# Optimization experiments

Hardware: AMD Instinct MI355X
Metric: run time of the kernel (lower is better)

Reference implementation:

```python
import jax, jax.numpy as jnp
import numpy as np

EPS = 1e-5  # torch LayerNorm default

def layer_norm(x, scale, bias):
    m = jnp.mean(x, axis=-1, keepdims=True)
    v = jnp.var(x, axis=-1, keepdims=True)
    return (x - m) * jax.lax.rsqrt(v + EPS) * scale + bias

def setup_inputs() -> dict:
    key = jax.random.key(0)
    ks = jax.random.split(key, 8)
    B, N, E, D = 2, 50000, 262144, 256
    node_features = jax.random.normal(ks[0], (B, N, D), jnp.float32)
    edge_index = jax.random.randint(ks[1], (B, E, 2), 0, N)
    edge_relations = jax.random.normal(ks[2], (B, E, D), jnp.float32)
    edge_mask = jnp.ones((B, E), jnp.float32)
    sc = 1.0 / np.sqrt(D).astype(np.float32)
    rel_w = jax.random.normal(ks[3], (D, D), jnp.float32) * sc
    rel_b = jnp.zeros((D,), jnp.float32)
    norm_s = jnp.ones((D,), jnp.float32)
    norm_b = jnp.zeros((D,), jnp.float32)
    w1 = jax.random.normal(ks[4], (D, 4 * D), jnp.float32) * sc
    b1 = jnp.zeros((4 * D,), jnp.float32)
    w2 = jax.random.normal(ks[5], (4 * D, D), jnp.float32) * (1.0 / np.sqrt(4 * D).astype(np.float32))
    b2 = jnp.zeros((D,), jnp.float32)
    ffn_s = jnp.ones((D,), jnp.float32)
    ffn_b = jnp.zeros((D,), jnp.float32)
    return dict(node_features=node_features, edge_relations=edge_relations,
                edge_mask=edge_mask, rel_w=rel_w, rel_b=rel_b,
                norm_s=norm_s, norm_b=norm_b, w1=w1, b1=b1, w2=w2, b2=b2,
                ffn_s=ffn_s, ffn_b=ffn_b, edge_index=edge_index)

def reference(node_features, edge_relations, edge_mask, rel_w, rel_b,
              norm_s, norm_b, w1, b1, w2, b2, ffn_s, ffn_b, edge_index):
    B, N, D = node_features.shape
    bidx = jnp.arange(B)[:, None]                      # [B,1] batch index for gather/scatter
    src_idx = edge_index[:, :, 0]                      # [B,E]
    tgt_idx = edge_index[:, :, 1]                      # [B,E]
    src_features = node_features[bidx, src_idx]        # gather -> [B,E,D]
    rel_features = edge_relations @ rel_w + rel_b      # [B,E,D]
    messages = (src_features + rel_features) * edge_mask[..., None]
    aggregated = jnp.zeros_like(node_features).at[bidx, tgt_idx].add(messages)
    counts = jnp.zeros((B, N, 1), node_features.dtype).at[bidx, tgt_idx].add(edge_mask[..., None])
    counts = jnp.maximum(counts, 1.0)
    aggregated = aggregated / counts
    x = layer_norm(node_features + aggregated, norm_s, norm_b)
    h = jax.nn.gelu(x @ w1 + b1, approximate=False)    # torch GELU default = exact erf
    x = layer_norm(x + (h @ w2 + b2), ffn_s, ffn_b)
    return x
```

## Files before the change

### kernel.cpp

```cpp
#include <hip/hip_runtime.h>
#include <math.h>

#define Bn 2
#define Nn 50000
#define En 262144
#define Dn 256
#define Hn 1024
#define RTOT (Bn*Nn)
#define RHALF 50000

typedef short bf16x8 __attribute__((ext_vector_type(8)));
typedef float f32x4 __attribute__((ext_vector_type(4)));

__device__ __forceinline__ short f2b(float f) {
  unsigned u = __float_as_uint(f);
  u = u + 0x7fffu + ((u >> 16) & 1u);
  return (short)(u >> 16);
}

__device__ __forceinline__ float gelu_f(float v) {
  float x = fabsf(v) * 0.70710678118654752f;
  float t = __builtin_amdgcn_rcpf(1.0f + 0.47047f * x);
  float p = t*(0.3480242f + t*(-0.0958798f + t*0.7478556f));
  float er = 1.0f - p * __expf(-x*x);
  er = copysignf(er, v);
  return 0.5f * v * (1.0f + er);
}

__device__ __forceinline__ void gl16(const void* g, void* l) {
  __builtin_amdgcn_global_load_lds(
      (const __attribute__((address_space(1))) unsigned int*)g,
      (__attribute__((address_space(3))) unsigned int*)l, 16, 0, 0);
}

__global__ void __launch_bounds__(256) wconv(
    const float* __restrict__ relw, const float* __restrict__ w1,
    const float* __restrict__ w2, short* __restrict__ relwT,
    short* __restrict__ w1s, short* __restrict__ w2s) {
  int tid = blockIdx.x * 256 + threadIdx.x;
  if (tid < Dn*Dn) { int c = tid >> 8, k = tid & 255; relwT[tid] = f2b(relw[k*Dn + c]); }
  int t1 = tid - Dn*Dn;
  if (t1 >= 0 && t1 < Dn*Hn) {
    int kk = t1 >> 16, rem = t1 & 65535;
    int col = rem >> 6, kl = rem & 63;
    w1s[kk*65536 + col*64 + (kl ^ ((col & 7) << 3))] = f2b(w1[(kk*64 + kl)*Hn + col]);
  }
  int t2 = tid - Dn*Dn - Dn*Hn;
  if (t2 >= 0 && t2 < Hn*Dn) {
    int kk = t2 >> 14, rem = t2 & 16383;
    int col = rem >> 6, kl = rem & 63;
    w2s[kk*16384 + col*64 + (kl ^ ((col & 7) << 3))] = f2b(w2[(kk*64 + kl)*Dn + col]);
  }
}

__global__ void __launch_bounds__(256) histk(const int* __restrict__ ei, int* __restrict__ cnt) {
  int tid = blockIdx.x * 256 + threadIdx.x;
  if (tid >= Bn*En) return;
  int b = tid / En;
  int tgt = ei[tid*2 + 1];
  atomicAdd(&cnt[b*Nn + tgt], 1);
}

__global__ void __launch_bounds__(256) offsk(const int* __restrict__ cnt,
                                             int* __restrict__ offs, int* __restrict__ gtot) {
  int i = blockIdx.x * 256 + threadIdx.x;
  int lane = threadIdx.x & 63;
  int v = (i < RTOT) ? cnt[i] : 0;
  int s = v;
#pragma unroll
  for (int d = 1; d < 64; d <<= 1) {
    int t = __shfl_up(s, d, 64);
    if (lane >= d) s += t;
  }
  int base = 0;
  if (lane == 63) base = atomicAdd(gtot, s);
  base = __shfl(base, 63, 64);
  if (i < RTOT) offs[i] = base + s - v;
}

__global__ void __launch_bounds__(256) fillk(const int* __restrict__ ei, const int* __restrict__ offs,
                                             int* __restrict__ cursor, int* __restrict__ eids) {
  int tid = blockIdx.x * 256 + threadIdx.x;
  if (tid >= Bn*En) return;
  int b = tid / En, e = tid - b*En;
  int tgt = ei[tid*2 + 1];
  int node = b*Nn + tgt;
  int pos = atomicAdd(&cursor[node], 1);
  eids[offs[node] + pos] = e;
}

__global__ void __launch_bounds__(256) aggk(
    const float* __restrict__ nodef, const float* __restrict__ erel,
    const float* __restrict__ emask, const int* __restrict__ ei,
    const int* __restrict__ offs, const int* __restrict__ cnt,
    const int* __restrict__ eids,
    float* __restrict__ sumrel, float* __restrict__ cntf, float* __restrict__ outsrc) {
  int w = (blockIdx.x * 256 + threadIdx.x) >> 6;
  int lane = threadIdx.x & 63;
  if (w >= RTOT) return;
  int b = w / Nn;
  const size_t ebase = (size_t)b * En;
  const size_t nbase = (size_t)b * Nn;
  int s0 = offs[w], s1 = s0 + cnt[w];
  float r0=0,r1=0,r2=0,r3=0, a0=0,a1=0,a2=0,a3=0, cf=0;
  for (int base = s0; base < s1; base += 64) {
    int k = s1 - base; if (k > 64) k = 64;
    int e = 0, sr = 0; float m = 0.f;
    if (lane < k) {
      e  = eids[base + lane];
      sr = ei[(ebase + e)*2];
      m  = emask[ebase + e];
    }
    int e0 = __shfl(e, 0), sr0 = __shfl(sr, 0);
    float m0 = __shfl(m, 0);
    float4 rvA = *(const float4*)(erel  + (ebase + e0)*Dn + lane*4);
    float4 nvA = *(const float4*)(nodef + (nbase + sr0)*Dn + lane*4);
    for (int j = 0; j < k; j++) {
      float4 rvB = make_float4(0,0,0,0), nvB = make_float4(0,0,0,0);
      float m1 = 0.f;
      if (j + 1 < k) {
        int e1 = __shfl(e, j+1), sr1 = __shfl(sr, j+1);
        m1 = __shfl(m, j+1);
        rvB = *(const float4*)(erel  + (ebase + e1)*Dn + lane*4);
        nvB = *(const float4*)(nodef + (nbase + sr1)*Dn + lane*4);
      }
      r0 += rvA.x*m0; r1 += rvA.y*m0; r2 += rvA.z*m0; r3 += rvA.w*m0;
      a0 += nvA.x*m0; a1 += nvA.y*m0; a2 += nvA.z*m0; a3 += nvA.w*m0;
      cf += m0;
      rvA = rvB; nvA = nvB; m0 = m1;
    }
  }
  size_t ob = (size_t)w*Dn + lane*4;
  *(float4*)(sumrel + ob) = make_float4(r0,r1,r2,r3);
  *(float4*)(outsrc + ob) = make_float4(a0,a1,a2,a3);
  if (lane == 0) cntf[w] = cf;
}

template<int MR>
__device__ __forceinline__ void stageX(const float* __restrict__ src, char* lds, int row0, int tid) {
#pragma unroll
  for (int i = 0; i < MR*4; i++) {
    int flat = tid + 256*i;
    int r = flat >> 6, c4 = flat & 63;
    float4 v = *(const float4*)(src + (size_t)(row0 + r)*Dn + c4*4);
    short4 s; s.x=f2b(v.x); s.y=f2b(v.y); s.z=f2b(v.z); s.w=f2b(v.w);
    int byte = r*512 + ((c4*8) ^ ((r & 7) << 4));
    *(short4*)(lds + byte) = s;
  }
}

__device__ __forceinline__ bf16x8 ldsA(const char* lds, int r, int kb) {
  int byte = r*512 + (((kb)*2) ^ ((r & 7) << 4));
  return *(const bf16x8*)(lds + byte);
}

template<int MR>
__device__ __forceinline__ void ln_write(f32x4 (&acc)[MR][4], float* red,
    const float* __restrict__ sc, const float* __restrict__ bi,
    float* __restrict__ out, int row0, int lane, int wv) {
  constexpr int R = MR*16;
  int l15 = lane & 15, l4 = lane >> 4;
  int cols[4]; float sc_c[4], bi_c[4];
#pragma unroll
  for (int n = 0; n < 4; n++) {
    cols[n] = wv*64 + n*16 + l15;
    sc_c[n] = sc[cols[n]]; bi_c[n] = bi[cols[n]];
  }
  float s1[MR][4], s2[MR][4];
#pragma unroll
  for (int m = 0; m < MR; m++)
#pragma unroll
    for (int g = 0; g < 4; g++) {
      float a = 0.f, b = 0.f;
#pragma unroll
      for (int n = 0; n < 4; n++) { float p = acc[m][n][g]; a += p; b += p*p; }
#pragma unroll
      for (int d = 1; d < 16; d <<= 1) { a += __shfl_xor(a, d, 16); b += __shfl_xor(b, d, 16); }
      s1[m][g] = a; s2[m][g] = b;
    }
  if (l15 == 0) {
#pragma unroll
    for (int m = 0; m < MR; m++)
#pragma unroll
      for (int g = 0; g < 4; g++) {
        int r = m*16 + l4*4 + g;
        red[(wv*R + r)*2]     = s1[m][g];
        red[(wv*R + r)*2 + 1] = s2[m][g];
      }
  }
  __syncthreads();
#pragma unroll
  for (int m = 0; m < MR; m++)
#pragma unroll
    for (int g = 0; g < 4; g++) {
      int r = m*16 + l4*4 + g; int rg = row0 + r;
      float t1 = 0.f, t2 = 0.f;
#pragma unroll
      for (int u = 0; u < 4; u++) { t1 += red[(u*R + r)*2]; t2 += red[(u*R + r)*2 + 1]; }
      float mean = t1 * (1.0f/Dn);
      float var  = t2 * (1.0f/Dn) - mean*mean;
      float rstd = rsqrtf(var + 1e-5f);
#pragma unroll
      for (int n = 0; n < 4; n++)
        out[(size_t)rg*Dn + cols[n]] = (acc[m][n][g] - mean)*rstd*sc_c[n] + bi_c[n];
    }
}

__global__ void __launch_bounds__(256, 4) relln(
    const float* __restrict__ sumrel, const short* __restrict__ relwT,
    const float* __restrict__ relb, const float* __restrict__ nodef,
    const float* __restrict__ cntf, const float* __restrict__ ns,
    const float* __restrict__ nb, float* __restrict__ xout) {
  constexpr int MR = 2;
  __shared__ __align__(16) char lds[16384 + 1024];
  float* red = (float*)(lds + 16384);
  int tid = threadIdx.x;
  int lane = tid & 63, wv = tid >> 6;
  int l15 = lane & 15, l4 = lane >> 4;
  int row0 = blockIdx.x * (MR*16);
  stageX<MR>(sumrel, lds, row0, tid);
  __syncthreads();
  f32x4 acc[MR][4] = {};
#pragma unroll
  for (int ks = 0; ks < 8; ks++) {
    bf16x8 af[MR], bfr[4];
#pragma unroll
    for (int m = 0; m < MR; m++) af[m] = ldsA(lds, m*16 + l15, ks*32 + l4*8);
#pragma unroll
    for (int n = 0; n < 4; n++) {
      int col = wv*64 + n*16 + l15;
      bfr[n] = *(const bf16x8*)(relwT + col*Dn + ks*32 + l4*8);
    }
#pragma unroll
    for (int m = 0; m < MR; m++)
#pragma unroll
      for (int n = 0; n < 4; n++)
        acc[m][n] = __builtin_amdgcn_mfma_f32_16x16x32_bf16(af[m], bfr[n], acc[m][n], 0, 0, 0);
  }
  int cols[4]; float rb_c[4];
#pragma unroll
  for (int n = 0; n < 4; n++) { cols[n] = wv*64 + n*16 + l15; rb_c[n] = relb[cols[n]]; }
#pragma unroll
  for (int m = 0; m < MR; m++)
#pragma unroll
    for (int g = 0; g < 4; g++) {
      int r = m*16 + l4*4 + g; int rg = row0 + r;
      float cf  = cntf[rg];
      float inv = 1.0f / fmaxf(cf, 1.0f);
#pragma unroll
      for (int n = 0; n < 4; n++) {
        float ssrc = xout[(size_t)rg*Dn + cols[n]];
        float nfv  = nodef[(size_t)rg*Dn + cols[n]];
        float aggv = (ssrc + acc[m][n][g] + cf*rb_c[n]) * inv;
        acc[m][n][g] = nfv + aggv;
      }
    }
  ln_write<MR>(acc, red, ns, nb, xout, row0, lane, wv);
}

__global__ void __launch_bounds__(512, 4) ffn1k(
    const float* __restrict__ x, const short* __restrict__ w1s,
    const float* __restrict__ b1, short* __restrict__ H, int gstart) {
  __shared__ __align__(16) char lds[32768];
  char* Xa = lds;
  char* W1a = lds + 16384;
  int tid = threadIdx.x;
  int lane = tid & 63, wv = tid >> 6;
  int l15 = lane & 15, l4 = lane >> 4;
  int wm = wv >> 2, wn = wv & 3;
  int row0 = blockIdx.x * 128;
  int col0 = blockIdx.y * 128;

  f32x4 acc[4][2] = {};
#pragma unroll 1
  for (int kk = 0; kk < 4; kk++) {
    {
      int r = tid >> 2, kb = (tid & 3) * 16;
      int gr = gstart + row0 + r;
      if (gr > RTOT - 1) gr = RTOT - 1;
      const float* p = x + (size_t)gr*Dn + kk*64 + kb;
      float4 v0 = *(const float4*)(p);
      float4 v1 = *(const float4*)(p + 4);
      float4 v2 = *(const float4*)(p + 8);
      float4 v3 = *(const float4*)(p + 12);
      bf16x8 s0, s1;
      s0[0]=f2b(v0.x); s0[1]=f2b(v0.y); s0[2]=f2b(v0.z); s0[3]=f2b(v0.w);
      s0[4]=f2b(v1.x); s0[5]=f2b(v1.y); s0[6]=f2b(v1.z); s0[7]=f2b(v1.w);
      s1[0]=f2b(v2.x); s1[1]=f2b(v2.y); s1[2]=f2b(v2.z); s1[3]=f2b(v2.w);
      s1[4]=f2b(v3.x); s1[5]=f2b(v3.y); s1[6]=f2b(v3.z); s1[7]=f2b(v3.w);
      *(bf16x8*)(Xa + r*128 + ((kb*2)      ^ ((r & 7) << 4))) = s0;
      *(bf16x8*)(Xa + r*128 + ((kb*2 + 16) ^ ((r & 7) << 4))) = s1;
    }
#pragma unroll
    for (int i = 0; i < 2; i++) {
      int base = wv*2048 + i*1024;
      gl16((const char*)w1s + (size_t)kk*131072 + col0*128 + base + lane*16,
           W1a + base + lane*16);
    }
    __syncthreads();
#pragma unroll
    for (int ksl = 0; ksl < 2; ksl++) {
      bf16x8 af[4], bw[2];
#pragma unroll
      for (int mf = 0; mf < 4; mf++) {
        int r = wm*64 + mf*16 + l15;
        af[mf] = *(const bf16x8*)(Xa + r*128 + (((ksl*32 + l4*8)*2) ^ ((r & 7) << 4)));
      }
#pragma unroll
      for (int nf = 0; nf < 2; nf++) {
        int c = wn*32 + nf*16 + l15;
        bw[nf] = *(const bf16x8*)(W1a + c*128 + (((ksl*32 + l4*8)*2) ^ ((c & 7) << 4)));
      }
#pragma unroll
      for (int mf = 0; mf < 4; mf++)
#pragma unroll
        for (int nf = 0; nf < 2; nf++)
          acc[mf][nf] = __builtin_amdgcn_mfma_f32_16x16x32_bf16(af[mf], bw[nf], acc[mf][nf], 0, 0, 0);
    }
    __syncthreads();
  }
  float b1v[2];
#pragma unroll
  for (int nf = 0; nf < 2; nf++) b1v[nf] = b1[col0 + wn*32 + nf*16 + l15];
#pragma unroll
  for (int mf = 0; mf < 4; mf++)
#pragma unroll
    for (int g = 0; g < 4; g++) {
      int R = wm*64 + mf*16 + l4*4 + g;
#pragma unroll
      for (int nf = 0; nf < 2; nf++) {
        int C = wn*32 + nf*16 + l15;
        float hv = gelu_f(acc[mf][nf][g] + b1v[nf]);
        *(short*)(lds + R*256 + ((C*2) ^ ((R & 7) << 4))) = f2b(hv);
      }
    }
  __syncthreads();
#pragma unroll
  for (int i = 0; i < 4; i++) {
    int flat = tid + i*512;
    int r = flat >> 4, c8 = (flat & 15) * 8;
    if (row0 + r >= RHALF) continue;
    bf16x8 v = *(const bf16x8*)(lds + r*256 + ((c8*2) ^ ((r & 7) << 4)));
    int gc = col0 + c8;
    size_t hb = (size_t)(row0 + r)*2048 + (gc >> 6)*128 + (((gc & 63)*2) ^ (((row0 + r) & 7) << 4));
    *(bf16x8*)((char*)H + hb) = v;
  }
}

__global__ void __launch_bounds__(512, 4) ffn2k(
    const short* __restrict__ H, const short* __restrict__ w2s,
    const float* __restrict__ b2, const float* __restrict__ fs,
    const float* __restrict__ fb, float* __restrict__ xio, int gstart) {
  __shared__ __align__(16) char lds[8192 + 32768];
  char* Ha  = lds;
  char* W2a = lds + 8192;
  float* red = (float*)lds;
  int tid = threadIdx.x;
  int lane = tid & 63, wv = tid >> 6;
  int l15 = lane & 15, l4 = lane >> 4;
  int wm = wv >> 2, wn = wv & 3;
  int rows0 = blockIdx.x * 64;

  f32x4 acc[2][4] = {};
#pragma unroll 1
  for (int kk = 0; kk < 16; kk++) {
    {
      int flat = wv*1024 + lane*16;
      int r = flat >> 7, bo = flat & 127;
      int lr = rows0 + r; if (lr > RHALF - 1) lr = RHALF - 1;
      gl16((const char*)H + (size_t)lr*2048 + kk*128 + bo, Ha + flat);
    }
#pragma unroll
    for (int i = 0; i < 4; i++) {
      int base = wv*4096 + i*1024;
      gl16((const char*)w2s + (size_t)kk*32768 + base + lane*16, W2a + base + lane*16);
    }
    __syncthreads();
#pragma unroll
    for (int ksl = 0; ksl < 2; ksl++) {
      bf16x8 ah[2], bw[4];
#pragma unroll
      for (int mf = 0; mf < 2; mf++) {
        int r = wm*32 + mf*16 + l15;
        ah[mf] = *(const bf16x8*)(Ha + r*128 + (((ksl*32 + l4*8)*2) ^ ((r & 7) << 4)));
      }
#pragma unroll
      for (int nf = 0; nf < 4; nf++) {
        int c = wn*64 + nf*16 + l15;
        bw[nf] = *(const bf16x8*)(W2a + c*128 + (((ksl*32 + l4*8)*2) ^ ((c & 7) << 4)));
      }
#pragma unroll
      for (int mf = 0; mf < 2; mf++)
#pragma unroll
        for (int nf = 0; nf < 4; nf++)
          acc[mf][nf] = __builtin_amdgcn_mfma_f32_16x16x32_bf16(ah[mf], bw[nf], acc[mf][nf], 0, 0, 0);
    }
    __syncthreads();
  }
  float b2c[4], fsc[4], fbc[4];
#pragma unroll
  for (int nf = 0; nf < 4; nf++) {
    int col = wn*64 + nf*16 + l15;
    b2c[nf] = b2[col]; fsc[nf] = fs[col]; fbc[nf] = fb[col];
  }
#pragma unroll
  for (int mf = 0; mf < 2; mf++)
#pragma unroll
    for (int g = 0; g < 4; g++) {
      int R = wm*32 + mf*16 + l4*4 + g;
      int lr = rows0 + R;
      bool ok = lr < RHALF;
      int gr = gstart + lr;
      float a = 0.f, q = 0.f;
#pragma unroll
      for (int nf = 0; nf < 4; nf++) {
        int col = wn*64 + nf*16 + l15;
        float xv = ok ? xio[(size_t)gr*Dn + col] : 0.f;
        float vv = xv + acc[mf][nf][g] + b2c[nf];
        acc[mf][nf][g] = vv;
        a += vv; q += vv*vv;
      }
#pragma unroll
      for (int d = 1; d < 16; d <<= 1) { a += __shfl_xor(a, d, 16); q += __shfl_xor(q, d, 16); }
      if (l15 == 0) {
        red[(wn*64 + R)*2]     = a;
        red[(wn*64 + R)*2 + 1] = q;
      }
    }
  __syncthreads();
#pragma unroll
  for (int mf = 0; mf < 2; mf++)
#pragma unroll
    for (int g = 0; g < 4; g++) {
      int R = wm*32 + mf*16 + l4*4 + g;
      int lr = rows0 + R;
      if (lr >= RHALF) continue;
      int gr = gstart + lr;
      float t1 = 0.f, t2 = 0.f;
#pragma unroll
      for (int u = 0; u < 4; u++) { t1 += red[(u*64 + R)*2]; t2 += red[(u*64 + R)*2 + 1]; }
      float mean = t1 * (1.0f/Dn);
      float var  = t2 * (1.0f/Dn) - mean*mean;
      float rstd = rsqrtf(var + 1e-5f);
#pragma unroll
      for (int nf = 0; nf < 4; nf++) {
        int col = wn*64 + nf*16 + l15;
        xio[(size_t)gr*Dn + col] = (acc[mf][nf][g] - mean)*rstd*fsc[nf] + fbc[nf];
      }
    }
}

extern "C" void kernel_launch(void* const* d_in, const int* in_sizes, int n_in,
                              void* d_out, int out_size, void* d_ws, size_t ws_size,
                              hipStream_t stream) {
  const float* nodef = (const float*)d_in[0];
  const float* erel  = (const float*)d_in[1];
  const float* emask = (const float*)d_in[2];
  const float* relw  = (const float*)d_in[3];
  const float* relb  = (const float*)d_in[4];
  const float* ns    = (const float*)d_in[5];
  const float* nb    = (const float*)d_in[6];
  const float* w1    = (const float*)d_in[7];
  const float* b1    = (const float*)d_in[8];
  const float* w2    = (const float*)d_in[9];
  const float* b2    = (const float*)d_in[10];
  const float* fs    = (const float*)d_in[11];
  const float* fb    = (const float*)d_in[12];
  const int*   ei    = (const int*)d_in[13];
  float* out = (float*)d_out;
  char* ws = (char*)d_ws;

  constexpr size_t SZ_SUMREL = (size_t)RTOT * Dn * 4;
  constexpr size_t O_CNT  = SZ_SUMREL;
  constexpr size_t O_CUR  = O_CNT + (size_t)RTOT*4;
  constexpr size_t O_OFF  = O_CUR + (size_t)RTOT*4;
  constexpr size_t O_EID  = O_OFF + ((size_t)(RTOT+1)*4 + 124);
  constexpr size_t O_CNTF = O_EID + (size_t)Bn*En*4;
  constexpr size_t O_RWT  = O_CNTF + (size_t)RTOT*4;
  constexpr size_t O_W1T  = O_RWT + (size_t)Dn*Dn*2;
  constexpr size_t O_W2T  = O_W1T + (size_t)Dn*Hn*2;
  constexpr size_t WS_NEED = O_W2T + (size_t)Hn*Dn*2;
  if (ws_size < WS_NEED) return;

  float* sumrel = (float*)(ws);
  short* Hbuf   = (short*)(ws);
  int*   cnt    = (int*)(ws + O_CNT);
  int*   cursor = (int*)(ws + O_CUR);
  int*   offs   = (int*)(ws + O_OFF);
  int*   eids   = (int*)(ws + O_EID);
  float* cntf   = (float*)(ws + O_CNTF);
  short* relwT  = (short*)(ws + O_RWT);
  short* w1s    = (short*)(ws + O_W1T);
  short* w2s    = (short*)(ws + O_W2T);
  int*   gtot   = offs + RTOT;

  hipMemsetAsync(ws + O_CNT, 0, O_EID - O_CNT, stream);

  wconv<<<(Dn*Dn + Dn*Hn + Hn*Dn + 255) / 256, 256, 0, stream>>>(relw, w1, w2, relwT, w1s, w2s);
  histk<<<(Bn*En) / 256, 256, 0, stream>>>(ei, cnt);
  offsk<<<(RTOT + 255) / 256, 256, 0, stream>>>(cnt, offs, gtot);
  fillk<<<(Bn*En) / 256, 256, 0, stream>>>(ei, offs, cursor, eids);
  aggk<<<(RTOT + 3) / 4, 256, 0, stream>>>(nodef, erel, emask, ei, offs, cnt, eids, sumrel, cntf, out);
  relln<<<RTOT / 32, 256, 0, stream>>>(sumrel, relwT, relb, nodef, cntf, ns, nb, out);

  dim3 g1((RHALF + 127) / 128, Hn / 128);
  int g2 = (RHALF + 63) / 64;
  for (int half = 0; half < 2; half++) {
    int gstart = half * RHALF;
    ffn1k<<<g1, 512, 0, stream>>>(out, w1s, b1, Hbuf, gstart);
    ffn2k<<<g2, 512, 0, stream>>>(Hbuf, w2s, b2, fs, fb, out, gstart);
  }
}
```

Before: 673.5 us.

## Store intermediates as bf16, widen FFN1 tiles, and drop the two-half FFN split

The aggregation kernel now processes two edges per wave using half-waves, reduces across halves, and writes the relation and source sums as swizzled bf16 rows. relln loads these rows straight into LDS with direct global-to-LDS loads, does the LayerNorm inline, and writes x as swizzled bf16. ffn1k reads that bf16 x directly and uses a 256-thread block with a 4x4 MFMA tile per wave. The FFN now runs once over all rows with a full-size H buffer instead of two halves. This cuts fp32 traffic and conversion work, at the cost of bf16 rounding on the residual x and a larger workspace.

Measured after the change: 633.2 us. -6.0%, faster.

```diff
diff --git a/kernel.cpp b/kernel.cpp
--- a/kernel.cpp
+++ b/kernel.cpp
@@ -7,7 +7,6 @@
 #define Dn 256
 #define Hn 1024
 #define RTOT (Bn*Nn)
-#define RHALF 50000
 
 typedef short bf16x8 __attribute__((ext_vector_type(8)));
 typedef float f32x4 __attribute__((ext_vector_type(4)));
@@ -16,6 +15,9 @@
   unsigned u = __float_as_uint(f);
   u = u + 0x7fffu + ((u >> 16) & 1u);
   return (short)(u >> 16);
+}
+__device__ __forceinline__ float b2f(unsigned short s) {
+  return __uint_as_float(((unsigned)s) << 16);
 }
 
 __device__ __forceinline__ float gelu_f(float v) {
@@ -94,59 +96,62 @@
     const float* __restrict__ emask, const int* __restrict__ ei,
     const int* __restrict__ offs, const int* __restrict__ cnt,
     const int* __restrict__ eids,
-    float* __restrict__ sumrel, float* __restrict__ cntf, float* __restrict__ outsrc) {
+    short* __restrict__ sumrelB, short* __restrict__ sumsrcB, float* __restrict__ cntf) {
   int w = (blockIdx.x * 256 + threadIdx.x) >> 6;
   int lane = threadIdx.x & 63;
   if (w >= RTOT) return;
   int b = w / Nn;
   const size_t ebase = (size_t)b * En;
   const size_t nbase = (size_t)b * Nn;
-  int s0 = offs[w], s1 = s0 + cnt[w];
-  float r0=0,r1=0,r2=0,r3=0, a0=0,a1=0,a2=0,a3=0, cf=0;
-  for (int base = s0; base < s1; base += 64) {
-    int k = s1 - base; if (k > 64) k = 64;
+  int s0 = offs[w], kall = cnt[w];
+  int h = lane >> 5, l32 = lane & 31;
+  float r[8] = {}, a[8] = {};
+  float cf = 0.f;
+  for (int base = 0; base < kall; base += 64) {
+    int k = kall - base; if (k > 64) k = 64;
     int e = 0, sr = 0; float m = 0.f;
     if (lane < k) {
-      e  = eids[base + lane];
+      e  = eids[s0 + base + lane];
       sr = ei[(ebase + e)*2];
       m  = emask[ebase + e];
     }
-    int e0 = __shfl(e, 0), sr0 = __shfl(sr, 0);
-    float m0 = __shfl(m, 0);
-    float4 rvA = *(const float4*)(erel  + (ebase + e0)*Dn + lane*4);
-    float4 nvA = *(const float4*)(nodef + (nbase + sr0)*Dn + lane*4);
-    for (int j = 0; j < k; j++) {
-      float4 rvB = make_float4(0,0,0,0), nvB = make_float4(0,0,0,0);
-      float m1 = 0.f;
-      if (j + 1 < k) {
-        int e1 = __shfl(e, j+1), sr1 = __shfl(sr, j+1);
-        m1 = __shfl(m, j+1);
-        rvB = *(const float4*)(erel  + (ebase + e1)*Dn + lane*4);
-        nvB = *(const float4*)(nodef + (nbase + sr1)*Dn + lane*4);
-      }
-      r0 += rvA.x*m0; r1 += rvA.y*m0; r2 += rvA.z*m0; r3 += rvA.w*m0;
-      a0 += nvA.x*m0; a1 += nvA.y*m0; a2 += nvA.z*m0; a3 += nvA.w*m0;
-      cf += m0;
-      rvA = rvB; nvA = nvB; m0 = m1;
-    }
-  }
-  size_t ob = (size_t)w*Dn + lane*4;
-  *(float4*)(sumrel + ob) = make_float4(r0,r1,r2,r3);
-  *(float4*)(outsrc + ob) = make_float4(a0,a1,a2,a3);
+    for (int j = 0; j < k; j += 2) {
+      int je = j + h;
+      int e1  = __shfl(e, je, 64);
+      int sr1 = __shfl(sr, je, 64);
+      float m1 = __shfl(m, je, 64);
+      if (je < k) {
+        const float* rp = erel  + (ebase + e1)*Dn + l32*8;
+        const float* np = nodef + (nbase + sr1)*Dn + l32*8;
+        float4 rv0 = *(const float4*)rp;
+        float4 rv1 = *(const float4*)(rp + 4);
+        float4 nv0 = *(const float4*)np;
+        float4 nv1 = *(const float4*)(np + 4);
+        r[0]+=rv0.x*m1; r[1]+=rv0.y*m1; r[2]+=rv0.z*m1; r[3]+=rv0.w*m1;
+        r[4]+=rv1.x*m1; r[5]+=rv1.y*m1; r[6]+=rv1.z*m1; r[7]+=rv1.w*m1;
+        a[0]+=nv0.x*m1; a[1]+=nv0.y*m1; a[2]+=nv0.z*m1; a[3]+=nv0.w*m1;
+        a[4]+=nv1.x*m1; a[5]+=nv1.y*m1; a[6]+=nv1.z*m1; a[7]+=nv1.w*m1;
+        cf += m1;
+      }
+    }
+  }
+#pragma unroll
+  for (int i = 0; i < 8; i++) {
+    r[i] += __shfl_xor(r[i], 32, 64);
+    a[i] += __shfl_xor(a[i], 32, 64);
+  }
+  cf += __shfl_xor(cf, 32, 64);
+  bf16x8 o;
+  if (h == 0) {
+#pragma unroll
+    for (int i = 0; i < 8; i++) o[i] = f2b(r[i]);
+    *(bf16x8*)((char*)sumrelB + (size_t)w*512 + ((l32*16) ^ ((w & 7) << 4))) = o;
+  } else {
+#pragma unroll
+    for (int i = 0; i < 8; i++) o[i] = f2b(a[i]);
+    *(bf16x8*)((char*)sumsrcB + (size_t)w*512 + l32*16) = o;
+  }
   if (lane == 0) cntf[w] = cf;
-}
-
-template<int MR>
-__device__ __forceinline__ void stageX(const float* __restrict__ src, char* lds, int row0, int tid) {
-#pragma unroll
-  for (int i = 0; i < MR*4; i++) {
-    int flat = tid + 256*i;
-    int r = flat >> 6, c4 = flat & 63;
-    float4 v = *(const float4*)(src + (size_t)(row0 + r)*Dn + c4*4);
-    short4 s; s.x=f2b(v.x); s.y=f2b(v.y); s.z=f2b(v.z); s.w=f2b(v.w);
-    int byte = r*512 + ((c4*8) ^ ((r & 7) << 4));
-    *(short4*)(lds + byte) = s;
-  }
 }
 
 __device__ __forceinline__ bf16x8 ldsA(const char* lds, int r, int kb) {
@@ -154,71 +159,25 @@
   return *(const bf16x8*)(lds + byte);
 }
 
-template<int MR>
-__device__ __forceinline__ void ln_write(f32x4 (&acc)[MR][4], float* red,
-    const float* __restrict__ sc, const float* __restrict__ bi,
-    float* __restrict__ out, int row0, int lane, int wv) {
-  constexpr int R = MR*16;
-  int l15 = lane & 15, l4 = lane >> 4;
-  int cols[4]; float sc_c[4], bi_c[4];
-#pragma unroll
-  for (int n = 0; n < 4; n++) {
-    cols[n] = wv*64 + n*16 + l15;
-    sc_c[n] = sc[cols[n]]; bi_c[n] = bi[cols[n]];
-  }
-  float s1[MR][4], s2[MR][4];
-#pragma unroll
-  for (int m = 0; m < MR; m++)
-#pragma unroll
-    for (int g = 0; g < 4; g++) {
-      float a = 0.f, b = 0.f;
-#pragma unroll
-      for (int n = 0; n < 4; n++) { float p = acc[m][n][g]; a += p; b += p*p; }
-#pragma unroll
-      for (int d = 1; d < 16; d <<= 1) { a += __shfl_xor(a, d, 16); b += __shfl_xor(b, d, 16); }
-      s1[m][g] = a; s2[m][g] = b;
-    }
-  if (l15 == 0) {
-#pragma unroll
-    for (int m = 0; m < MR; m++)
-#pragma unroll
-      for (int g = 0; g < 4; g++) {
-        int r = m*16 + l4*4 + g;
-        red[(wv*R + r)*2]     = s1[m][g];
-        red[(wv*R + r)*2 + 1] = s2[m][g];
-      }
-  }
-  __syncthreads();
-#pragma unroll
-  for (int m = 0; m < MR; m++)
-#pragma unroll
-    for (int g = 0; g < 4; g++) {
-      int r = m*16 + l4*4 + g; int rg = row0 + r;
-      float t1 = 0.f, t2 = 0.f;
-#pragma unroll
-      for (int u = 0; u < 4; u++) { t1 += red[(u*R + r)*2]; t2 += red[(u*R + r)*2 + 1]; }
-      float mean = t1 * (1.0f/Dn);
-      float var  = t2 * (1.0f/Dn) - mean*mean;
-      float rstd = rsqrtf(var + 1e-5f);
-#pragma unroll
-      for (int n = 0; n < 4; n++)
-        out[(size_t)rg*Dn + cols[n]] = (acc[m][n][g] - mean)*rstd*sc_c[n] + bi_c[n];
-    }
-}
-
 __global__ void __launch_bounds__(256, 4) relln(
-    const float* __restrict__ sumrel, const short* __restrict__ relwT,
+    const short* __restrict__ sumrelB, const short* __restrict__ relwT,
     const float* __restrict__ relb, const float* __restrict__ nodef,
-    const float* __restrict__ cntf, const float* __restrict__ ns,
-    const float* __restrict__ nb, float* __restrict__ xout) {
+    const short* __restrict__ sumsrcB, const float* __restrict__ cntf,
+    const float* __restrict__ ns, const float* __restrict__ nb,
+    short* __restrict__ xb) {
   constexpr int MR = 2;
   __shared__ __align__(16) char lds[16384 + 1024];
   float* red = (float*)(lds + 16384);
   int tid = threadIdx.x;
   int lane = tid & 63, wv = tid >> 6;
   int l15 = lane & 15, l4 = lane >> 4;
-  int row0 = blockIdx.x * (MR*16);
-  stageX<MR>(sumrel, lds, row0, tid);
+  int row0 = blockIdx.x * 32;
+#pragma unroll
+  for (int i = 0; i < 4; i++) {
+    int u = tid + 256*i;
+    int r = u >> 5, wb = (u & 31) * 16;
+    gl16((const char*)sumrelB + (size_t)(row0 + r)*512 + wb, lds + u*16);
+  }
   __syncthreads();
   f32x4 acc[MR][4] = {};
 #pragma unroll
@@ -237,9 +196,13 @@
       for (int n = 0; n < 4; n++)
         acc[m][n] = __builtin_amdgcn_mfma_f32_16x16x32_bf16(af[m], bfr[n], acc[m][n], 0, 0, 0);
   }
-  int cols[4]; float rb_c[4];
-#pragma unroll
-  for (int n = 0; n < 4; n++) { cols[n] = wv*64 + n*16 + l15; rb_c[n] = relb[cols[n]]; }
+  int cols[4]; float rb_c[4], ns_c[4], nb_c[4];
+#pragma unroll
+  for (int n = 0; n < 4; n++) {
+    cols[n] = wv*64 + n*16 + l15;
+    rb_c[n] = relb[cols[n]]; ns_c[n] = ns[cols[n]]; nb_c[n] = nb[cols[n]];
+  }
+  float s1[MR][4], s2[MR][4];
 #pragma unroll
   for (int m = 0; m < MR; m++)
 #pragma unroll
@@ -247,102 +210,125 @@
       int r = m*16 + l4*4 + g; int rg = row0 + r;
       float cf  = cntf[rg];
       float inv = 1.0f / fmaxf(cf, 1.0f);
+      float aa = 0.f, qq = 0.f;
 #pragma unroll
       for (int n = 0; n < 4; n++) {
-        float ssrc = xout[(size_t)rg*Dn + cols[n]];
+        float ssrc = b2f(*(const unsigned short*)((const char*)sumsrcB + (size_t)rg*512 + cols[n]*2));
         float nfv  = nodef[(size_t)rg*Dn + cols[n]];
-        float aggv = (ssrc + acc[m][n][g] + cf*rb_c[n]) * inv;
-        acc[m][n][g] = nfv + aggv;
-      }
-    }
-  ln_write<MR>(acc, red, ns, nb, xout, row0, lane, wv);
-}
-
-__global__ void __launch_bounds__(512, 4) ffn1k(
-    const float* __restrict__ x, const short* __restrict__ w1s,
-    const float* __restrict__ b1, short* __restrict__ H, int gstart) {
+        float vv = nfv + (ssrc + acc[m][n][g] + cf*rb_c[n]) * inv;
+        acc[m][n][g] = vv;
+        aa += vv; qq += vv*vv;
+      }
+#pragma unroll
+      for (int d = 1; d < 16; d <<= 1) { aa += __shfl_xor(aa, d, 16); qq += __shfl_xor(qq, d, 16); }
+      s1[m][g] = aa; s2[m][g] = qq;
+    }
+  if (l15 == 0) {
+#pragma unroll
+    for (int m = 0; m < MR; m++)
+#pragma unroll
+      for (int g = 0; g < 4; g++) {
+        int r = m*16 + l4*4 + g;
+        red[(wv*32 + r)*2]     = s1[m][g];
+        red[(wv*32 + r)*2 + 1] = s2[m][g];
+      }
+  }
+  __syncthreads();
+#pragma unroll
+  for (int m = 0; m < MR; m++)
+#pragma unroll
+    for (int g = 0; g < 4; g++) {
+      int r = m*16 + l4*4 + g; int rg = row0 + r;
+      float t1 = 0.f, t2 = 0.f;
+#pragma unroll
+      for (int u = 0; u < 4; u++) { t1 += red[(u*32 + r)*2]; t2 += red[(u*32 + r)*2 + 1]; }
+      float mean = t1 * (1.0f/Dn);
+      float var  = t2 * (1.0f/Dn) - mean*mean;
+      float rstd = rsqrtf(var + 1e-5f);
+#pragma unroll
+      for (int n = 0; n < 4; n++) {
+        float xv = (acc[m][n][g] - mean)*rstd*ns_c[n] + nb_c[n];
+        *(short*)((char*)xb + (size_t)rg*512 + ((cols[n]*2) ^ ((rg & 7) << 4))) = f2b(xv);
+      }
+    }
+}
+
+__global__ void __launch_bounds__(256) ffn1k(
+    const short* __restrict__ xb, const short* __restrict__ w1s,
+    const float* __restrict__ b1, short* __restrict__ H) {
   __shared__ __align__(16) char lds[32768];
   char* Xa = lds;
-  char* W1a = lds + 16384;
+  char* Wa = lds + 16384;
   int tid = threadIdx.x;
   int lane = tid & 63, wv = tid >> 6;
   int l15 = lane & 15, l4 = lane >> 4;
-  int wm = wv >> 2, wn = wv & 3;
+  int wm = wv >> 1, wn = wv & 1;
   int row0 = blockIdx.x * 128;
   int col0 = blockIdx.y * 128;
 
-  f32x4 acc[4][2] = {};
+  f32x4 acc[4][4] = {};
 #pragma unroll 1
   for (int kk = 0; kk < 4; kk++) {
-    {
-      int r = tid >> 2, kb = (tid & 3) * 16;
-      int gr = gstart + row0 + r;
-      if (gr > RTOT - 1) gr = RTOT - 1;
-      const float* p = x + (size_t)gr*Dn + kk*64 + kb;
-      float4 v0 = *(const float4*)(p);
-      float4 v1 = *(const float4*)(p + 4);
-      float4 v2 = *(const float4*)(p + 8);
-      float4 v3 = *(const float4*)(p + 12);
-      bf16x8 s0, s1;
-      s0[0]=f2b(v0.x); s0[1]=f2b(v0.y); s0[2]=f2b(v0.z); s0[3]=f2b(v0.w);
-      s0[4]=f2b(v1.x); s0[5]=f2b(v1.y); s0[6]=f2b(v1.z); s0[7]=f2b(v1.w);
-      s1[0]=f2b(v2.x); s1[1]=f2b(v2.y); s1[2]=f2b(v2.z); s1[3]=f2b(v2.w);
-      s1[4]=f2b(v3.x); s1[5]=f2b(v3.y); s1[6]=f2b(v3.z); s1[7]=f2b(v3.w);
-      *(bf16x8*)(Xa + r*128 + ((kb*2)      ^ ((r & 7) << 4))) = s0;
-      *(bf16x8*)(Xa + r*128 + ((kb*2 + 16) ^ ((r & 7) << 4))) = s1;
-    }
-#pragma unroll
-    for (int i = 0; i < 2; i++) {
-      int base = wv*2048 + i*1024;
-      gl16((const char*)w1s + (size_t)kk*131072 + col0*128 + base + lane*16,
-           W1a + base + lane*16);
+#pragma unroll
+    for (int i = 0; i < 4; i++) {
+      int u = tid + 256*i;
+      int r = u >> 3, wb = (u & 7) * 16;
+      int gr = row0 + r; if (gr > RTOT - 1) gr = RTOT - 1;
+      gl16((const char*)xb + (size_t)gr*512 + kk*128 + wb, Xa + u*16);
+    }
+#pragma unroll
+    for (int i = 0; i < 4; i++) {
+      int u = tid + 256*i;
+      gl16((const char*)w1s + (size_t)kk*131072 + col0*128 + u*16, Wa + u*16);
     }
     __syncthreads();
 #pragma unroll
     for (int ksl = 0; ksl < 2; ksl++) {
-      bf16x8 af[4], bw[2];
+      int kb2 = (ksl*32 + l4*8) * 2;
+      bf16x8 af[4], bw[4];
 #pragma unroll
       for (int mf = 0; mf < 4; mf++) {
         int r = wm*64 + mf*16 + l15;
-        af[mf] = *(const bf16x8*)(Xa + r*128 + (((ksl*32 + l4*8)*2) ^ ((r & 7) << 4)));
-      }
-#pragma unroll
-      for (int nf = 0; nf < 2; nf++) {
-        int c = wn*32 + nf*16 + l15;
-        bw[nf] = *(const bf16x8*)(W1a + c*128 + (((ksl*32 + l4*8)*2) ^ ((c & 7) << 4)));
+        af[mf] = *(const bf16x8*)(Xa + r*128 + (kb2 ^ ((r & 7) << 4)));
+      }
+#pragma unroll
+      for (int nf = 0; nf < 4; nf++) {
+        int c = wn*64 + nf*16 + l15;
+        bw[nf] = *(const bf16x8*)(Wa + c*128 + (kb2 ^ ((c & 7) << 4)));
       }
 #pragma unroll
       for (int mf = 0; mf < 4; mf++)
 #pragma unroll
-        for (int nf = 0; nf < 2; nf++)
+        for (int nf = 0; nf < 4; nf++)
           acc[mf][nf] = __builtin_amdgcn_mfma_f32_16x16x32_bf16(af[mf], bw[nf], acc[mf][nf], 0, 0, 0);
     }
     __syncthreads();
   }
-  float b1v[2];
-#pragma unroll
-  for (int nf = 0; nf < 2; nf++) b1v[nf] = b1[col0 + wn*32 + nf*16 + l15];
+  float b1v[4];
+#pragma unroll
+  for (int nf = 0; nf < 4; nf++) b1v[nf] = b1[col0 + wn*64 + nf*16 + l15];
 #pragma unroll
   for (int mf = 0; mf < 4; mf++)
 #pragma unroll
     for (int g = 0; g < 4; g++) {
       int R = wm*64 + mf*16 + l4*4 + g;
 #pragma unroll
-      for (int nf = 0; nf < 2; nf++) {
-        int C = wn*32 + nf*16 + l15;
+      for (int nf = 0; nf < 4; nf++) {
+        int C = wn*64 + nf*16 + l15;
         float hv = gelu_f(acc[mf][nf][g] + b1v[nf]);
         *(short*)(lds + R*256 + ((C*2) ^ ((R & 7) << 4))) = f2b(hv);
       }
     }
   __syncthreads();
 #pragma unroll
-  for (int i = 0; i < 4; i++) {
-    int flat = tid + i*512;
-    int r = flat >> 4, c8 = (flat & 15) * 8;
-    if (row0 + r >= RHALF) continue;
-    bf16x8 v = *(const bf16x8*)(lds + r*256 + ((c8*2) ^ ((r & 7) << 4)));
-    int gc = col0 + c8;
-    size_t hb = (size_t)(row0 + r)*2048 + (gc >> 6)*128 + (((gc & 63)*2) ^ (((row0 + r) & 7) << 4));
+  for (int i = 0; i < 8; i++) {
+    int u = tid + 256*i;
+    int r = u >> 4, c = (u & 15) * 8;
+    int gr = row0 + r;
+    if (gr >= RTOT) continue;
+    bf16x8 v = *(const bf16x8*)(lds + r*256 + ((c*2) ^ ((r & 7) << 4)));
+    int gc = col0 + c;
+    size_t hb = (size_t)gr*2048 + (gc >> 6)*128 + (((gc & 63)*2) ^ ((gr & 7) << 4));
     *(bf16x8*)((char*)H + hb) = v;
   }
 }
@@ -350,7 +336,8 @@
 __global__ void __launch_bounds__(512, 4) ffn2k(
     const short* __restrict__ H, const short* __restrict__ w2s,
     const float* __restrict__ b2, const float* __restrict__ fs,
-    const float* __restrict__ fb, float* __restrict__ xio, int gstart) {
+    const float* __restrict__ fb, const short* __restrict__ xb,
+    float* __restrict__ out) {
   __shared__ __align__(16) char lds[8192 + 32768];
   char* Ha  = lds;
   char* W2a = lds + 8192;
@@ -367,7 +354,7 @@
     {
       int flat = wv*1024 + lane*16;
       int r = flat >> 7, bo = flat & 127;
-      int lr = rows0 + r; if (lr > RHALF - 1) lr = RHALF - 1;
+      int lr = rows0 + r; if (lr > RTOT - 1) lr = RTOT - 1;
       gl16((const char*)H + (size_t)lr*2048 + kk*128 + bo, Ha + flat);
     }
 #pragma unroll
@@ -408,14 +395,14 @@
 #pragma unroll
     for (int g = 0; g < 4; g++) {
       int R = wm*32 + mf*16 + l4*4 + g;
-      int lr = rows0 + R;
-      bool ok = lr < RHALF;
-      int gr = gstart + lr;
+      int gr = rows0 + R;
+      bool ok = gr < RTOT;
       float a = 0.f, q = 0.f;
 #pragma unroll
       for (int nf = 0; nf < 4; nf++) {
         int col = wn*64 + nf*16 + l15;
-        float xv = ok ? xio[(size_t)gr*Dn + col] : 0.f;
+        float xv = 0.f;
+        if (ok) xv = b2f(*(const unsigned short*)((const char*)xb + (size_t)gr*512 + ((col*2) ^ ((gr & 7) << 4))));
         float vv = xv + acc[mf][nf][g] + b2c[nf];
         acc[mf][nf][g] = vv;
         a += vv; q += vv*vv;
@@ -433,9 +420,8 @@
 #pragma unroll
     for (int g = 0; g < 4; g++) {
       int R = wm*32 + mf*16 + l4*4 + g;
-      int lr = rows0 + R;
-      if (lr >= RHALF) continue;
-      int gr = gstart + lr;
+      int gr = rows0 + R;
+      if (gr >= RTOT) continue;
       float t1 = 0.f, t2 = 0.f;
 #pragma unroll
       for (int u = 0; u < 4; u++) { t1 += red[(u*64 + R)*2]; t2 += red[(u*64 + R)*2 + 1]; }
@@ -445,7 +431,7 @@
 #pragma unroll
       for (int nf = 0; nf < 4; nf++) {
         int col = wn*64 + nf*16 + l15;
-        xio[(size_t)gr*Dn + col] = (acc[mf][nf][g] - mean)*rstd*fsc[nf] + fbc[nf];
+        out[(size_t)gr*Dn + col] = (acc[mf][nf][g] - mean)*rstd*fsc[nf] + fbc[nf];
       }
     }
 }
@@ -470,20 +456,26 @@
   float* out = (float*)d_out;
   char* ws = (char*)d_ws;
 
-  constexpr size_t SZ_SUMREL = (size_t)RTOT * Dn * 4;
-  constexpr size_t O_CNT  = SZ_SUMREL;
-  constexpr size_t O_CUR  = O_CNT + (size_t)RTOT*4;
-  constexpr size_t O_OFF  = O_CUR + (size_t)RTOT*4;
-  constexpr size_t O_EID  = O_OFF + ((size_t)(RTOT+1)*4 + 124);
+  constexpr size_t SZ_ROWB = (size_t)RTOT * Dn * 2;
+  constexpr size_t O_SRB = 0;
+  constexpr size_t O_SSB = O_SRB + SZ_ROWB;
+  constexpr size_t O_XB  = O_SSB + SZ_ROWB;
+  constexpr size_t O_H   = O_XB + SZ_ROWB;
+  constexpr size_t O_CNT = O_H + (size_t)RTOT * Hn * 2;
+  constexpr size_t O_CUR = O_CNT + (size_t)RTOT*4;
+  constexpr size_t O_OFF = O_CUR + (size_t)RTOT*4;
+  constexpr size_t O_EID = O_OFF + ((size_t)(RTOT+1)*4 + 124);
   constexpr size_t O_CNTF = O_EID + (size_t)Bn*En*4;
-  constexpr size_t O_RWT  = O_CNTF + (size_t)RTOT*4;
-  constexpr size_t O_W1T  = O_RWT + (size_t)Dn*Dn*2;
-  constexpr size_t O_W2T  = O_W1T + (size_t)Dn*Hn*2;
+  constexpr size_t O_RWT = O_CNTF + (size_t)RTOT*4;
+  constexpr size_t O_W1T = O_RWT + (size_t)Dn*Dn*2;
+  constexpr size_t O_W2T = O_W1T + (size_t)Dn*Hn*2;
   constexpr size_t WS_NEED = O_W2T + (size_t)Hn*Dn*2;
   if (ws_size < WS_NEED) return;
 
-  float* sumrel = (float*)(ws);
-  short* Hbuf   = (short*)(ws);
+  short* sumrelB = (short*)(ws + O_SRB);
+  short* sumsrcB = (short*)(ws + O_SSB);
+  short* xb      = (short*)(ws + O_XB);
+  short* Hbuf    = (short*)(ws + O_H);
   int*   cnt    = (int*)(ws + O_CNT);
   int*   cursor = (int*)(ws + O_CUR);
   int*   offs   = (int*)(ws + O_OFF);
@@ -500,14 +492,9 @@
   histk<<<(Bn*En) / 256, 256, 0, stream>>>(ei, cnt);
   offsk<<<(RTOT + 255) / 256, 256, 0, stream>>>(cnt, offs, gtot);
   fillk<<<(Bn*En) / 256, 256, 0, stream>>>(ei, offs, cursor, eids);
-  aggk<<<(RTOT + 3) / 4, 256, 0, stream>>>(nodef, erel, emask, ei, offs, cnt, eids, sumrel, cntf, out);
-  relln<<<RTOT / 32, 256, 0, stream>>>(sumrel, relwT, relb, nodef, cntf, ns, nb, out);
-
-  dim3 g1((RHALF + 127) / 128, Hn / 128);
-  int g2 = (RHALF + 63) / 64;
-  for (int half = 0; half < 2; half++) {
-    int gstart = half * RHALF;
-    ffn1k<<<g1, 512, 0, stream>>>(out, w1s, b1, Hbuf, gstart);
-    ffn2k<<<g2, 512, 0, stream>>>(Hbuf, w2s, b2, fs, fb, out, gstart);
-  }
-}
+  aggk<<<(RTOT + 3) / 4, 256, 0, stream>>>(nodef, erel, emask, ei, offs, cnt, eids,
+                                           sumrelB, sumsrcB, cntf);
+  relln<<<RTOT / 32, 256, 0, stream>>>(sumrelB, relwT, relb, nodef, sumsrcB, cntf, ns, nb, xb);
+  ffn1k<<<dim3((RTOT + 127) / 128, Hn / 128), 256, 0, stream>>>(xb, w1s, b1, Hbuf);
+  ffn2k<<<(RTOT + 63) / 64, 512, 0, stream>>>(Hbuf, w2s, b2, fs, fb, xb, out);
+}
```
